# Optimization experiments

Hardware: AMD Instinct MI355X
Metric: run time of the kernel (lower is better)

Reference implementation:

```python
import jax, jax.numpy as jnp
import numpy as np

B = 1048576
H = 16  # LSTM hidden size

def setup_inputs() -> dict:
    key = jax.random.key(0)
    ks = jax.random.split(key, 16)
    s = 1.0 / np.sqrt(H)
    return {
        "mobility": jax.random.normal(ks[0], (B, 7, 1), dtype=jnp.float32),
        "controls": jax.random.normal(ks[1], (B, 5), dtype=jnp.float32),
        "last": jax.random.normal(ks[2], (B, 1), dtype=jnp.float32),
        # cc: Linear(5 -> 3)
        "W_cc": jax.random.uniform(ks[3], (3, 5), jnp.float32, -s, s),
        "b_cc": jax.random.uniform(ks[4], (3,), jnp.float32, -s, s),
        # LSTM(input=1, hidden=16), gate order i,f,g,o
        "W_ih": jax.random.uniform(ks[5], (4 * H, 1), jnp.float32, -s, s),
        "W_hh": jax.random.uniform(ks[6], (4 * H, H), jnp.float32, -s, s),
        "b_ih": jax.random.uniform(ks[7], (4 * H,), jnp.float32, -s, s),
        "b_hh": jax.random.uniform(ks[8], (4 * H,), jnp.float32, -s, s),
        # fc: Linear(19->16), Tanh, Dropout(eval=identity), Linear(16->16), Tanh, Linear(16->1), ReLU
        "W1": jax.random.uniform(ks[9], (16, 19), jnp.float32, -s, s),
        "b1": jax.random.uniform(ks[10], (16,), jnp.float32, -s, s),
        "W2": jax.random.uniform(ks[11], (16, 16), jnp.float32, -s, s),
        "b2": jax.random.uniform(ks[12], (16,), jnp.float32, -s, s),
        "W3": jax.random.uniform(ks[13], (1, 16), jnp.float32, -s, s),
        "b3": jax.random.uniform(ks[14], (1,), jnp.float32, -s, s),
    }

def _lstm(x, W_ih, W_hh, b_ih, b_hh):
    # x: [B, T, 1] -> final hidden state [B, H]
    b = x.shape[0]
    h0 = jnp.zeros((b, H), x.dtype)
    c0 = jnp.zeros((b, H), x.dtype)
    bias = b_ih + b_hh

    def step(carry, x_t):
        h, c = carry
        gates = x_t @ W_ih.T + h @ W_hh.T + bias  # [B, 4H]
        i, f, g, o = jnp.split(gates, 4, axis=-1)
        i = jax.nn.sigmoid(i)
        f = jax.nn.sigmoid(f)
        g = jnp.tanh(g)
        o = jax.nn.sigmoid(o)
        c = f * c + i * g
        h = o * jnp.tanh(c)
        return (h, c), None

    (h, c), _ = jax.lax.scan(step, (h0, c0), jnp.swapaxes(x, 0, 1))
    return h

def reference(mobility, controls, last, W_cc, b_cc, W_ih, W_hh, b_ih, b_hh, W1, b1, W2, b2, W3, b3):
    control = controls @ W_cc.T + b_cc                 # [B, 3]
    m = _lstm(mobility, W_ih, W_hh, b_ih, b_hh)        # [B, 16] final hidden
    x = jnp.concatenate([m, control], axis=1)          # [B, 19]
    x = jnp.tanh(x @ W1.T + b1)                        # dropout is identity (eval)
    x = jnp.tanh(x @ W2.T + b2)
    out = jax.nn.relu(x @ W3.T + b3)                   # [B, 1]
    return out
```

## Files before the change

### kernel.cpp

```cpp
#include <hip/hip_runtime.h>
#include <hip/hip_bf16.h>

typedef _Float16 f16x8  __attribute__((ext_vector_type(8)));
typedef _Float16 f16x16 __attribute__((ext_vector_type(16)));
typedef float    f32x16 __attribute__((ext_vector_type(16)));
typedef float    v2f    __attribute__((ext_vector_type(2)));
typedef unsigned u32x4  __attribute__((ext_vector_type(4)));

#define LOG2E 1.442695040888963f

__device__ __forceinline__ unsigned pk16(float a, float b) {
    return __builtin_bit_cast(unsigned, __builtin_amdgcn_cvt_pkrtz(a, b));
}
__device__ __forceinline__ float fexp2(float x) { return __builtin_amdgcn_exp2f(x); }

__global__ __launch_bounds__(256, 3) void lstm_mfma_kernel(
    const float* __restrict__ mobility,
    const float* __restrict__ controls,
    const float* __restrict__ W_cc, const float* __restrict__ b_cc,
    const float* __restrict__ W_ih, const float* __restrict__ W_hh,
    const float* __restrict__ b_ih, const float* __restrict__ b_hh,
    const float* __restrict__ W1,  const float* __restrict__ b1,
    const float* __restrict__ W2,  const float* __restrict__ b2,
    const float* __restrict__ W3,  const float* __restrict__ b3,
    float* __restrict__ out, int Btot)
{
    __shared__ float hbuf[256][17];

    const int tid  = threadIdx.x;
    const int lane = tid & 63;
    const int wib  = tid >> 6;
    const int col  = lane & 31;
    const int hi   = lane >> 5;

    f16x8 afrag[2];
    #pragma unroll
    for (int gb = 0; gb < 2; ++gb) {
        const float s = (gb == 0) ? -LOG2E : ((col < 16) ? 2.0f * LOG2E : -LOG2E);
        const float* wr = W_hh + (gb * 32 + col) * 16 + hi * 8;
        u32x4 aw = { pk16(s * wr[0], s * wr[1]), pk16(s * wr[2], s * wr[3]),
                     pk16(s * wr[4], s * wr[5]), pk16(s * wr[6], s * wr[7]) };
        afrag[gb] = __builtin_bit_cast(f16x8, aw);
    }
    f16x16 bias_h[2], wih_h[2];
    #pragma unroll
    for (int gb = 0; gb < 2; ++gb)
        #pragma unroll
        for (int q = 0; q < 4; ++q) {
            const int gu = gb * 32 + 8 * q + 4 * hi;
            const float s = (gu < 32) ? -LOG2E : ((gu < 48) ? 2.0f * LOG2E : -LOG2E);
            #pragma unroll
            for (int e = 0; e < 4; ++e) {
                bias_h[gb][4 * q + e] = (_Float16)(s * (b_ih[gu + e] + b_hh[gu + e]));
                wih_h [gb][4 * q + e] = (_Float16)(s * W_ih[gu + e]);
            }
        }

    const v2f one   = { 1.0f, 1.0f };
    const v2f twoL  = { 2.0f * LOG2E, 2.0f * LOG2E };
    const v2f ntwoL = { -2.0f * LOG2E, -2.0f * LOG2E };

    const int tilesTotal = (Btot + 255) >> 8;
    for (int tile = blockIdx.x; tile < tilesTotal; tile += gridDim.x) {
        const int blockRow0 = tile * 256;
        const int r_lo = blockRow0 + wib * 64 + col;
        const int r_hi = r_lo + 32;

        float mlo[7], mhi[7];
        #pragma unroll
        for (int t = 0; t < 7; ++t) { mlo[t] = mobility[(size_t)r_lo * 7 + t]; mhi[t] = mobility[(size_t)r_hi * 7 + t]; }

        float c[2][8];
        #pragma unroll
        for (int rb = 0; rb < 2; ++rb)
            #pragma unroll
            for (int u = 0; u < 8; ++u) c[rb][u] = 0.0f;

        u32x4 bz = { 0u, 0u, 0u, 0u };
        f16x8 bfrag[2];
        bfrag[0] = __builtin_bit_cast(f16x8, bz);
        bfrag[1] = __builtin_bit_cast(f16x8, bz);

        #pragma unroll 1
        for (int t = 0; t < 7; ++t) {
            #pragma unroll
            for (int rb = 0; rb < 2; ++rb) {
                const float xt = rb ? mhi[t] : mlo[t];

                f32x16 cin0, cin1;
                #pragma unroll
                for (int r = 0; r < 16; ++r)
                    cin0[r] = fmaf(xt, (float)wih_h[0][r], (float)bias_h[0][r]);
                f32x16 a0 = __builtin_amdgcn_mfma_f32_32x32x16_f16(afrag[0], bfrag[rb], cin0, 0, 0, 0);
                #pragma unroll
                for (int r = 0; r < 16; ++r)
                    cin1[r] = fmaf(xt, (float)wih_h[1][r], (float)bias_h[1][r]);
                f32x16 a1 = __builtin_amdgcn_mfma_f32_32x32x16_f16(afrag[1], bfrag[rb], cin1, 0, 0, 0);

                float h[8];
                #pragma unroll
                for (int u = 0; u < 8; u += 2) {
                    v2f ea = { fexp2(a0[u]),     fexp2(a0[u + 1]) };
                    v2f ef = { fexp2(a0[u + 8]), fexp2(a0[u + 9]) };
                    v2f eb = { fexp2(a1[u]),     fexp2(a1[u + 1]) };
                    v2f eo = { fexp2(a1[u + 8]), fexp2(a1[u + 9]) };
                    v2f pf  = one + ef;
                    v2f pa  = one + ea;
                    v2f den = __builtin_elementwise_fma(pa, eb, pa);
                    v2f D   = den * pf;
                    v2f num = __builtin_elementwise_fma(eb, twoL, ntwoL);
                    v2f cv  = { c[rb][u], c[rb][u + 1] };
                    v2f cn  = __builtin_elementwise_fma(cv, den, num * pf);
                    const float rC = __builtin_amdgcn_rcpf(D[0] * D[1]);
                    v2f Dsw = { D[1], D[0] };
                    v2f rCv = { rC, rC };
                    v2f cs  = (cn * Dsw) * rCv;
                    c[rb][u]     = cs[0];
                    c[rb][u + 1] = cs[1];
                    v2f ec = { fexp2(cs[0]), fexp2(cs[1]) };
                    v2f ph = one + eo;
                    v2f dh = __builtin_elementwise_fma(ph, ec, ph);
                    v2f nh = ec - one;
                    const float rP = __builtin_amdgcn_rcpf(dh[0] * dh[1]);
                    v2f dsw = { dh[1], dh[0] };
                    v2f rPv = { rP, rP };
                    v2f hv  = (nh * dsw) * rPv;
                    h[u]     = hv[0];
                    h[u + 1] = hv[1];
                }
                unsigned q0 = pk16(h[0], h[1]);
                unsigned q1 = pk16(h[2], h[3]);
                unsigned q2 = pk16(h[4], h[5]);
                unsigned q3 = pk16(h[6], h[7]);
                auto s02 = __builtin_amdgcn_permlane32_swap(q0, q2, false, false);
                auto s13 = __builtin_amdgcn_permlane32_swap(q1, q3, false, false);
                u32x4 bw = { s02[0], s13[0], s02[1], s13[1] };
                bfrag[rb] = __builtin_bit_cast(f16x8, bw);
            }
        }

        #pragma unroll
        for (int rb = 0; rb < 2; ++rb) {
            const int rr = wib * 64 + col + rb * 32;
            #pragma unroll
            for (int e = 0; e < 8; ++e)
                hbuf[rr][hi * 8 + e] = (float)bfrag[rb][e];
        }
        __syncthreads();

        const int grow = blockRow0 + tid;

        float x19[19];
        #pragma unroll
        for (int k = 0; k < 16; ++k) x19[k] = hbuf[tid][k];

        float ctl[5];
        #pragma unroll
        for (int k = 0; k < 5; ++k) ctl[k] = controls[(size_t)grow * 5 + k];
        #pragma unroll
        for (int j = 0; j < 3; ++j) {
            float a = b_cc[j];
            #pragma unroll
            for (int k = 0; k < 5; ++k) a = fmaf(ctl[k], W_cc[j * 5 + k], a);
            x19[16 + j] = a;
        }

        float d1[16];
        #pragma unroll
        for (int j = 0; j < 16; ++j) {
            float a = b1[j];
            #pragma unroll
            for (int k = 0; k < 19; ++k) a = fmaf(x19[k], W1[j * 19 + k], a);
            d1[j] = fexp2((2.0f * LOG2E) * a) + 1.0f;
        }
        v2f t12[8];
        #pragma unroll
        for (int j = 0; j < 16; j += 2) {
            const float rP = __builtin_amdgcn_rcpf(d1[j] * d1[j + 1]);
            t12[j >> 1][0] = fmaf(-2.0f * d1[j + 1], rP, 1.0f);
            t12[j >> 1][1] = fmaf(-2.0f * d1[j],     rP, 1.0f);
        }

        float d2[16];
        #pragma unroll
        for (int j = 0; j < 16; ++j) {
            const v2f* w2row = (const v2f*)(W2 + j * 16);
            v2f a = t12[0] * w2row[0];
            #pragma unroll
            for (int p = 1; p < 8; ++p) a = __builtin_elementwise_fma(t12[p], w2row[p], a);
            d2[j] = fexp2((2.0f * LOG2E) * (a.x + a.y + b2[j])) + 1.0f;
        }
        v2f t22[8];
        #pragma unroll
        for (int j = 0; j < 16; j += 2) {
            const float rP = __builtin_amdgcn_rcpf(d2[j] * d2[j + 1]);
            t22[j >> 1][0] = fmaf(-2.0f * d2[j + 1], rP, 1.0f);
            t22[j >> 1][1] = fmaf(-2.0f * d2[j],     rP, 1.0f);
        }

        const v2f* w3p = (const v2f*)W3;
        v2f a3 = t22[0] * w3p[0];
        #pragma unroll
        for (int p = 1; p < 8; ++p) a3 = __builtin_elementwise_fma(t22[p], w3p[p], a3);
        const float r = a3.x + a3.y + b3[0];
        if (grow < Btot) out[grow] = fmaxf(r, 0.0f);

        __syncthreads();
    }
}

extern "C" void kernel_launch(void* const* d_in, const int* in_sizes, int n_in,
                              void* d_out, int out_size, void* d_ws, size_t ws_size,
                              hipStream_t stream) {
    const float* mobility = (const float*)d_in[0];
    const float* controls = (const float*)d_in[1];
    const float* W_cc = (const float*)d_in[3];
    const float* b_cc = (const float*)d_in[4];
    const float* W_ih = (const float*)d_in[5];
    const float* W_hh = (const float*)d_in[6];
    const float* b_ih = (const float*)d_in[7];
    const float* b_hh = (const float*)d_in[8];
    const float* W1   = (const float*)d_in[9];
    const float* b1   = (const float*)d_in[10];
    const float* W2   = (const float*)d_in[11];
    const float* b2   = (const float*)d_in[12];
    const float* W3   = (const float*)d_in[13];
    const float* b3   = (const float*)d_in[14];
    float* out = (float*)d_out;

    const int Btot  = in_sizes[0] / 7;
    const int tiles = (Btot + 255) / 256;
    const int grid  = tiles < 1024 ? tiles : 1024;

    lstm_mfma_kernel<<<grid, 256, 0, stream>>>(
        mobility, controls, W_cc, b_cc, W_ih, W_hh, b_ih, b_hh,
        W1, b1, W2, b2, W3, b3, out, Btot);
}
```

Before: 113.9 us.

## Move input projection and MLP head onto MFMA, drop LDS transpose

```diff
diff --git a/kernel.cpp b/kernel.cpp
--- a/kernel.cpp
+++ b/kernel.cpp
@@ -2,7 +2,6 @@
 #include <hip/hip_bf16.h>
 
 typedef _Float16 f16x8  __attribute__((ext_vector_type(8)));
-typedef _Float16 f16x16 __attribute__((ext_vector_type(16)));
 typedef float    f32x16 __attribute__((ext_vector_type(16)));
 typedef float    v2f    __attribute__((ext_vector_type(2)));
 typedef unsigned u32x4  __attribute__((ext_vector_type(4)));
@@ -13,6 +12,7 @@
     return __builtin_bit_cast(unsigned, __builtin_amdgcn_cvt_pkrtz(a, b));
 }
 __device__ __forceinline__ float fexp2(float x) { return __builtin_amdgcn_exp2f(x); }
+__device__ __forceinline__ float frcp(float x)  { return __builtin_amdgcn_rcpf(x); }
 
 __global__ __launch_bounds__(256, 3) void lstm_mfma_kernel(
     const float* __restrict__ mobility,
@@ -25,40 +25,64 @@
     const float* __restrict__ W3,  const float* __restrict__ b3,
     float* __restrict__ out, int Btot)
 {
-    __shared__ float hbuf[256][17];
-
     const int tid  = threadIdx.x;
     const int lane = tid & 63;
     const int wib  = tid >> 6;
     const int col  = lane & 31;
     const int hi   = lane >> 5;
 
-    f16x8 afrag[2];
+    const float S2 = 2.0f * LOG2E;
+
+    f16x8 afrag[2], afrag2[2];
     #pragma unroll
     for (int gb = 0; gb < 2; ++gb) {
-        const float s = (gb == 0) ? -LOG2E : ((col < 16) ? 2.0f * LOG2E : -LOG2E);
+        const float s = (gb == 0) ? -LOG2E : ((col < 16) ? S2 : -LOG2E);
         const float* wr = W_hh + (gb * 32 + col) * 16 + hi * 8;
         u32x4 aw = { pk16(s * wr[0], s * wr[1]), pk16(s * wr[2], s * wr[3]),
                      pk16(s * wr[4], s * wr[5]), pk16(s * wr[6], s * wr[7]) };
         afrag[gb] = __builtin_bit_cast(f16x8, aw);
+        u32x4 a2 = { 0u, 0u, 0u, 0u };
+        if (hi == 0) {
+            const int gu = gb * 32 + col;
+            a2[0] = pk16(s * W_ih[gu], s * (b_ih[gu] + b_hh[gu]));
+        }
+        afrag2[gb] = __builtin_bit_cast(f16x8, a2);
     }
-    f16x16 bias_h[2], wih_h[2];
+
+    f16x8 a_fc1, a_fc1c, a_fc2;
+    {
+        u32x4 w1 = {0u,0u,0u,0u}, w1c = {0u,0u,0u,0u}, w2 = {0u,0u,0u,0u};
+        if (col < 16) {
+            const float* r1 = W1 + col * 19 + hi * 8;
+            w1 = { pk16(S2*r1[0], S2*r1[1]), pk16(S2*r1[2], S2*r1[3]),
+                   pk16(S2*r1[4], S2*r1[5]), pk16(S2*r1[6], S2*r1[7]) };
+            const float* r2 = W2 + col * 16 + hi * 8;
+            w2 = { pk16(S2*r2[0], S2*r2[1]), pk16(S2*r2[2], S2*r2[3]),
+                   pk16(S2*r2[4], S2*r2[5]), pk16(S2*r2[6], S2*r2[7]) };
+            if (hi == 0) {
+                const float wa = W1[col*19+16], wb = W1[col*19+17], wc = W1[col*19+18];
+                float cc[5];
+                #pragma unroll
+                for (int k = 0; k < 5; ++k)
+                    cc[k] = wa * W_cc[0*5+k] + wb * W_cc[1*5+k] + wc * W_cc[2*5+k];
+                const float bp = b1[col] + wa * b_cc[0] + wb * b_cc[1] + wc * b_cc[2];
+                w1c = { pk16(S2*cc[0], S2*cc[1]), pk16(S2*cc[2], S2*cc[3]),
+                        pk16(S2*cc[4], S2*bp), 0u };
+            }
+        }
+        a_fc1  = __builtin_bit_cast(f16x8, w1);
+        a_fc1c = __builtin_bit_cast(f16x8, w1c);
+        a_fc2  = __builtin_bit_cast(f16x8, w2);
+    }
+    const float b3v = b3[0];
+
+    f32x16 fzero;
     #pragma unroll
-    for (int gb = 0; gb < 2; ++gb)
-        #pragma unroll
-        for (int q = 0; q < 4; ++q) {
-            const int gu = gb * 32 + 8 * q + 4 * hi;
-            const float s = (gu < 32) ? -LOG2E : ((gu < 48) ? 2.0f * LOG2E : -LOG2E);
-            #pragma unroll
-            for (int e = 0; e < 4; ++e) {
-                bias_h[gb][4 * q + e] = (_Float16)(s * (b_ih[gu + e] + b_hh[gu + e]));
-                wih_h [gb][4 * q + e] = (_Float16)(s * W_ih[gu + e]);
-            }
-        }
+    for (int r = 0; r < 16; ++r) fzero[r] = 0.0f;
 
     const v2f one   = { 1.0f, 1.0f };
-    const v2f twoL  = { 2.0f * LOG2E, 2.0f * LOG2E };
-    const v2f ntwoL = { -2.0f * LOG2E, -2.0f * LOG2E };
+    const v2f twoL  = { S2, S2 };
+    const v2f ntwoL = { -S2, -S2 };
 
     const int tilesTotal = (Btot + 255) >> 8;
     for (int tile = blockIdx.x; tile < tilesTotal; tile += gridDim.x) {
@@ -87,15 +111,14 @@
             for (int rb = 0; rb < 2; ++rb) {
                 const float xt = rb ? mhi[t] : mlo[t];
 
-                f32x16 cin0, cin1;
-                #pragma unroll
-                for (int r = 0; r < 16; ++r)
-                    cin0[r] = fmaf(xt, (float)wih_h[0][r], (float)bias_h[0][r]);
-                f32x16 a0 = __builtin_amdgcn_mfma_f32_32x32x16_f16(afrag[0], bfrag[rb], cin0, 0, 0, 0);
-                #pragma unroll
-                for (int r = 0; r < 16; ++r)
-                    cin1[r] = fmaf(xt, (float)wih_h[1][r], (float)bias_h[1][r]);
-                f32x16 a1 = __builtin_amdgcn_mfma_f32_32x32x16_f16(afrag[1], bfrag[rb], cin1, 0, 0, 0);
+                u32x4 b2w = { 0u, 0u, 0u, 0u };
+                if (hi == 0) b2w[0] = pk16(xt, 1.0f);
+                const f16x8 bx = __builtin_bit_cast(f16x8, b2w);
+
+                f32x16 acc0 = __builtin_amdgcn_mfma_f32_32x32x16_f16(afrag2[0], bx, fzero, 0, 0, 0);
+                f32x16 a0   = __builtin_amdgcn_mfma_f32_32x32x16_f16(afrag[0], bfrag[rb], acc0, 0, 0, 0);
+                f32x16 acc1 = __builtin_amdgcn_mfma_f32_32x32x16_f16(afrag2[1], bx, fzero, 0, 0, 0);
+                f32x16 a1   = __builtin_amdgcn_mfma_f32_32x32x16_f16(afrag[1], bfrag[rb], acc1, 0, 0, 0);
 
                 float h[8];
                 #pragma unroll
@@ -111,7 +134,7 @@
                     v2f num = __builtin_elementwise_fma(eb, twoL, ntwoL);
                     v2f cv  = { c[rb][u], c[rb][u + 1] };
                     v2f cn  = __builtin_elementwise_fma(cv, den, num * pf);
-                    const float rC = __builtin_amdgcn_rcpf(D[0] * D[1]);
+                    const float rC = frcp(D[0] * D[1]);
                     v2f Dsw = { D[1], D[0] };
                     v2f rCv = { rC, rC };
                     v2f cs  = (cn * Dsw) * rCv;
@@ -121,7 +144,7 @@
                     v2f ph = one + eo;
                     v2f dh = __builtin_elementwise_fma(ph, ec, ph);
                     v2f nh = ec - one;
-                    const float rP = __builtin_amdgcn_rcpf(dh[0] * dh[1]);
+                    const float rP = frcp(dh[0] * dh[1]);
                     v2f dsw = { dh[1], dh[0] };
                     v2f rPv = { rP, rP };
                     v2f hv  = (nh * dsw) * rPv;
@@ -139,73 +162,67 @@
             }
         }
 
+        float b2L[8], w3v[8];
+        #pragma unroll
+        for (int e = 0; e < 8; ++e) {
+            const int m = (e & 3) + 8 * (e >> 2) + 4 * hi;
+            b2L[e] = S2 * b2[m];
+            w3v[e] = W3[m];
+        }
+
         #pragma unroll
         for (int rb = 0; rb < 2; ++rb) {
-            const int rr = wib * 64 + col + rb * 32;
-            #pragma unroll
-            for (int e = 0; e < 8; ++e)
-                hbuf[rr][hi * 8 + e] = (float)bfrag[rb][e];
-        }
-        __syncthreads();
-
-        const int grow = blockRow0 + tid;
-
-        float x19[19];
-        #pragma unroll
-        for (int k = 0; k < 16; ++k) x19[k] = hbuf[tid][k];
-
-        float ctl[5];
-        #pragma unroll
-        for (int k = 0; k < 5; ++k) ctl[k] = controls[(size_t)grow * 5 + k];
-        #pragma unroll
-        for (int j = 0; j < 3; ++j) {
-            float a = b_cc[j];
-            #pragma unroll
-            for (int k = 0; k < 5; ++k) a = fmaf(ctl[k], W_cc[j * 5 + k], a);
-            x19[16 + j] = a;
-        }
-
-        float d1[16];
-        #pragma unroll
-        for (int j = 0; j < 16; ++j) {
-            float a = b1[j];
-            #pragma unroll
-            for (int k = 0; k < 19; ++k) a = fmaf(x19[k], W1[j * 19 + k], a);
-            d1[j] = fexp2((2.0f * LOG2E) * a) + 1.0f;
-        }
-        v2f t12[8];
-        #pragma unroll
-        for (int j = 0; j < 16; j += 2) {
-            const float rP = __builtin_amdgcn_rcpf(d1[j] * d1[j + 1]);
-            t12[j >> 1][0] = fmaf(-2.0f * d1[j + 1], rP, 1.0f);
-            t12[j >> 1][1] = fmaf(-2.0f * d1[j],     rP, 1.0f);
-        }
-
-        float d2[16];
-        #pragma unroll
-        for (int j = 0; j < 16; ++j) {
-            const v2f* w2row = (const v2f*)(W2 + j * 16);
-            v2f a = t12[0] * w2row[0];
-            #pragma unroll
-            for (int p = 1; p < 8; ++p) a = __builtin_elementwise_fma(t12[p], w2row[p], a);
-            d2[j] = fexp2((2.0f * LOG2E) * (a.x + a.y + b2[j])) + 1.0f;
-        }
-        v2f t22[8];
-        #pragma unroll
-        for (int j = 0; j < 16; j += 2) {
-            const float rP = __builtin_amdgcn_rcpf(d2[j] * d2[j + 1]);
-            t22[j >> 1][0] = fmaf(-2.0f * d2[j + 1], rP, 1.0f);
-            t22[j >> 1][1] = fmaf(-2.0f * d2[j],     rP, 1.0f);
-        }
-
-        const v2f* w3p = (const v2f*)W3;
-        v2f a3 = t22[0] * w3p[0];
-        #pragma unroll
-        for (int p = 1; p < 8; ++p) a3 = __builtin_elementwise_fma(t22[p], w3p[p], a3);
-        const float r = a3.x + a3.y + b3[0];
-        if (grow < Btot) out[grow] = fmaxf(r, 0.0f);
-
-        __syncthreads();
+            const int grow = rb ? r_hi : r_lo;
+            const float* ctl = controls + (size_t)grow * 5;
+
+            u32x4 bcw = { 0u, 0u, 0u, 0u };
+            if (hi == 0) {
+                bcw[0] = pk16(ctl[0], ctl[1]);
+                bcw[1] = pk16(ctl[2], ctl[3]);
+                bcw[2] = pk16(ctl[4], 1.0f);
+            }
+            const f16x8 bc = __builtin_bit_cast(f16x8, bcw);
+
+            f32x16 acc = __builtin_amdgcn_mfma_f32_32x32x16_f16(a_fc1c, bc, fzero, 0, 0, 0);
+            acc = __builtin_amdgcn_mfma_f32_32x32x16_f16(a_fc1, bfrag[rb], acc, 0, 0, 0);
+
+            float t1[8];
+            #pragma unroll
+            for (int r = 0; r < 8; r += 2) {
+                const float d0 = fexp2(acc[r])     + 1.0f;
+                const float d1 = fexp2(acc[r + 1]) + 1.0f;
+                const float rP = frcp(d0 * d1);
+                t1[r]     = fmaf(-2.0f * d1, rP, 1.0f);
+                t1[r + 1] = fmaf(-2.0f * d0, rP, 1.0f);
+            }
+            unsigned q0 = pk16(t1[0], t1[1]);
+            unsigned q1 = pk16(t1[2], t1[3]);
+            unsigned q2 = pk16(t1[4], t1[5]);
+            unsigned q3 = pk16(t1[6], t1[7]);
+            auto s02 = __builtin_amdgcn_permlane32_swap(q0, q2, false, false);
+            auto s13 = __builtin_amdgcn_permlane32_swap(q1, q3, false, false);
+            u32x4 bw = { s02[0], s13[0], s02[1], s13[1] };
+            const f16x8 bt1 = __builtin_bit_cast(f16x8, bw);
+
+            f32x16 acc2 = __builtin_amdgcn_mfma_f32_32x32x16_f16(a_fc2, bt1, fzero, 0, 0, 0);
+
+            float t2[8];
+            #pragma unroll
+            for (int r = 0; r < 8; r += 2) {
+                const float d0 = fexp2(acc2[r]     + b2L[r])     + 1.0f;
+                const float d1 = fexp2(acc2[r + 1] + b2L[r + 1]) + 1.0f;
+                const float rP = frcp(d0 * d1);
+                t2[r]     = fmaf(-2.0f * d1, rP, 1.0f);
+                t2[r + 1] = fmaf(-2.0f * d0, rP, 1.0f);
+            }
+
+            float dot = t2[0] * w3v[0];
+            #pragma unroll
+            for (int e = 1; e < 8; ++e) dot = fmaf(t2[e], w3v[e], dot);
+            const float tot = dot + __shfl_xor(dot, 32);
+            const float res = fmaxf(tot + b3v, 0.0f);
+            if (hi == 0 && grow < Btot) out[grow] = res;
+        }
     }
 }
 
```

After: 103.5 us. 1.1x faster.
